# Kernel optimization log

Hardware: AMD Instinct MI355X
Metric: run time of the kernel (lower is better)

Reference implementation:

```python
import jax, jax.numpy as jnp
import numpy as np

D = 512      # input_dim == encoder d_model
E = 512      # embedding_dim (codebook dim)
V = 8192     # num_embeddings
NC = 1       # num_codebooks
L = 6        # encoder layers
H = 8        # heads
F = 2048     # ffn dim
HD = D // H
EPS = 1e-5


def layernorm(x, s, b):
    m = jnp.mean(x, -1, keepdims=True)
    v = jnp.mean((x - m) ** 2, -1, keepdims=True)
    return (x - m) * jax.lax.rsqrt(v + EPS) * s + b


def sinusoidal_pe(T):
    pos = np.arange(T, dtype=np.float32)[:, None]
    i = np.arange(0, D, 2, dtype=np.float32)[None, :]
    ang = pos / np.power(10000.0, i / D)
    pe = np.zeros((T, D), np.float32)
    pe[:, 0::2] = np.sin(ang)
    pe[:, 1::2] = np.cos(ang)
    return jnp.asarray(pe)


def setup_inputs():
    key = jax.random.key(0)
    ks = jax.random.split(key, 12)
    B, T = 8, 1024
    xs = jax.random.normal(ks[0], (B, T, D), jnp.float32)
    xs_lens = (T // 2 + jax.random.randint(ks[1], (B,), 0, T // 2)).astype(jnp.int32)
    mask_indices = jax.random.uniform(ks[2], (B, T)) < 0.12  # span-mask surrogate
    sc = lambda k, shape, s=0.02: jax.random.normal(k, shape, jnp.float32) * s
    return {
        "xs": xs, "xs_lens": xs_lens, "mask_indices": mask_indices,
        "W_embed": sc(ks[3], (D, D), D ** -0.5),
        "ln1_s": jnp.ones((L, D)), "ln1_b": jnp.zeros((L, D)),
        "Wqkv": sc(ks[4], (L, D, 3 * D)), "Wo": sc(ks[5], (L, D, D)),
        "ln2_s": jnp.ones((L, D)), "ln2_b": jnp.zeros((L, D)),
        "W1": sc(ks[6], (L, D, F)), "W2": sc(ks[7], (L, F, D)),
        "an_s": jnp.ones((D,)), "an_b": jnp.zeros((D,)),
        "iln_s": jnp.ones((D,)), "iln_b": jnp.zeros((D,)),
        "mask_emb": sc(ks[8], (D,), 0.1),
        "top_n_out": sc(ks[9], (NC, D, V)),
        "projection": sc(ks[10], (D, E), (2.0 / (D + E)) ** 0.5),  # xavier_normal, frozen
        "embeddings": jax.random.normal(ks[11], (NC, E, V), jnp.float32),  # frozen codebook
    }


def encoder_blocks(x, pad_mask, ln1_s, ln1_b, Wqkv, Wo, ln2_s, ln2_b, W1, W2, an_s, an_b):
    B, T, _ = x.shape
    attn_bias = jnp.where(pad_mask, 0.0, -1e9)[:, None, None, :]  # [B,1,1,T]

    def layer(x, p):
        l1s, l1b, wqkv, wo, l2s, l2b, w1, w2 = p
        h = layernorm(x, l1s, l1b)
        q, k, v = jnp.split(h @ wqkv, 3, axis=-1)
        q = q.reshape(B, T, H, HD)
        k = k.reshape(B, T, H, HD)
        v = v.reshape(B, T, H, HD)
        scores = jnp.einsum('bqhd,bkhd->bhqk', q, k) * (HD ** -0.5) + attn_bias
        o = jnp.einsum('bhqk,bkhd->bqhd', jax.nn.softmax(scores, axis=-1), v)
        x = x + o.reshape(B, T, D) @ wo
        h = layernorm(x, l2s, l2b)
        x = x + jax.nn.relu(h @ w1) @ w2
        return x, None

    x, _ = jax.lax.scan(layer, x, (ln1_s, ln1_b, Wqkv, Wo, ln2_s, ln2_b, W1, W2))
    return layernorm(x, an_s, an_b)


def nearest_ids(x, iln_s, iln_b, projection, embeddings):
    # layernorm -> projection -> squared-distance argmin per codebook
    B, T, _ = x.shape
    z = layernorm(x, iln_s, iln_b) @ projection        # [B,T,E]
    flat = z.reshape(-1, E)                            # [N,E]
    d = (jnp.sum(flat ** 2, 1)[None, :, None]
         + jnp.sum(embeddings ** 2, 1)[:, None, :]
         - 2.0 * jnp.einsum('ne,gev->gnv', flat, embeddings))  # [NC,N,V]
    return jnp.argmin(d, -1).T.reshape(B, T, NC)


def reference(xs, xs_lens, mask_indices, W_embed, ln1_s, ln1_b, Wqkv, Wo, ln2_s, ln2_b,
              W1, W2, an_s, an_b, iln_s, iln_b, mask_emb, top_n_out, projection, embeddings):
    B, T, _ = xs.shape
    pad_mask = jnp.arange(T)[None, :] < xs_lens[:, None]              # [B,T]
    x = xs @ W_embed + sinusoidal_pe(T)[None]                         # encoder.embed
    target_ids = nearest_ids(x, iln_s, iln_b, projection, embeddings)  # [B,T,NC]
    masked_xs = jnp.where(mask_indices[..., None], mask_emb, x)
    out = encoder_blocks(masked_xs, pad_mask, ln1_s, ln1_b, Wqkv, Wo,
                         ln2_s, ln2_b, W1, W2, an_s, an_b)            # [B,T,D]
    logits = jnp.einsum('btd,gdv->bgtv', out, top_n_out)              # [B,NC,T,V]
    lsm = jax.nn.log_softmax(logits, axis=-1)
    tgt = jnp.transpose(target_ids, (0, 2, 1))                        # [B,NC,T]
    ent = -jnp.take_along_axis(lsm, tgt[..., None], axis=-1)[..., 0]  # [B,NC,T]
    m = (pad_mask & mask_indices).astype(jnp.float32)                 # [B,T]
    loss = jnp.sum(ent * m[:, None, :]) / (jnp.sum(m) * NC)
    return loss
```

## Files before the change

kernel.cpp:

```cpp
#include <hip/hip_runtime.h>
#include <hip/hip_bf16.h>

#define D_ 512
#define T_ 1024
#define B_ 8
#define H_ 8
#define F_ 2048
#define V_ 8192
#define L_ 6
#define NTOK 8192
#define EPS_ 1e-5f
#define NCAP 2048

typedef short short8 __attribute__((ext_vector_type(8)));
typedef float floatx4 __attribute__((ext_vector_type(4)));

__device__ __forceinline__ float bf2f(unsigned short u) {
  union { unsigned int i; float f; } v; v.i = ((unsigned int)u) << 16; return v.f;
}
__device__ __forceinline__ unsigned short f2bf(float f) {
  unsigned int u = __float_as_uint(f);
  return (unsigned short)((u + 0x7fffu + ((u >> 16) & 1u)) >> 16);
}
__device__ __forceinline__ float ldf(const void* p, long long i, int bf) {
  if (bf) return bf2f(((const unsigned short*)p)[i]);
  return ((const float*)p)[i];
}
__device__ __forceinline__ void ld16(const unsigned short* g, unsigned short* l) {
  __builtin_amdgcn_global_load_lds(
      (const __attribute__((address_space(1))) unsigned int*)g,
      (__attribute__((address_space(3))) unsigned int*)l, 16, 0, 0);
}
__device__ __forceinline__ unsigned int fkey(float f) {
  unsigned int u = __float_as_uint(f);
  return (u & 0x80000000u) ? ~u : (u ^ 0x80000000u);
}

__global__ void detect_kernel(const unsigned int* xsw, const unsigned int* mw, int* flags) {
  __shared__ int cnt[256];
  __shared__ int m01[256], mlo[256], mhi[256];
  int tid = threadIdx.x;
  int c = 0;
  for (int t = tid; t < 1024; t += 256) {
    unsigned int lo = xsw[t] & 0xffffu;
    int ok;
    if (lo == 0u) ok = 1;
    else { unsigned int e = (lo >> 7) & 0xffu; ok = (e >= 90u && e <= 140u); }
    c += ok;
  }
  int n01 = 0, lo38 = 0, hi38 = 0;
  for (int t = tid; t < 2048; t += 256) {
    unsigned int w = mw[t];
    if (w > 1u) n01 = 1;
    if ((w & 0xffffu) == 0x3f80u) lo38 = 1;
    if ((w >> 16) == 0x3f80u) hi38 = 1;
  }
  cnt[tid] = c; m01[tid] = n01; mlo[tid] = lo38; mhi[tid] = hi38;
  __syncthreads();
  for (int s = 128; s > 0; s >>= 1) {
    if (tid < s) {
      cnt[tid] += cnt[tid + s];
      m01[tid] |= m01[tid + s]; mlo[tid] |= mlo[tid + s]; mhi[tid] |= mhi[tid + s];
    }
    __syncthreads();
  }
  if (tid == 0) {
    flags[0] = (cnt[0] > 700) ? 1 : 0;
    int fmt;
    if (!m01[0]) fmt = 0;
    else if (mlo[0]) fmt = 2;
    else if (mhi[0]) fmt = 3;
    else fmt = 1;
    flags[1] = fmt;
  }
}

__global__ void conv_all_kernel(const void* d4, const void* d5, const void* d8,
                                const void* d9, const void* d12, const void* d13,
                                const void* d14, const void* d15, const void* d16,
                                float* P, const int* flags) {
  int i = blockIdx.x * 256 + threadIdx.x;
  if (i >= 14848) return;
  int bf = flags[0];
  const void* src; int off;
  if (i < 3072) { src = d4; off = 0; }
  else if (i < 6144) { src = d5; off = 3072; }
  else if (i < 9216) { src = d8; off = 6144; }
  else if (i < 12288) { src = d9; off = 9216; }
  else if (i < 12800) { src = d12; off = 12288; }
  else if (i < 13312) { src = d13; off = 12800; }
  else if (i < 13824) { src = d14; off = 13312; }
  else if (i < 14336) { src = d15; off = 13824; }
  else { src = d16; off = 14336; }
  P[i] = ldf(src, i - off, bf);
}

__global__ void convb_kernel(const void* src, unsigned short* dst, int n, const int* flags) {
  int i = blockIdx.x * 256 + threadIdx.x;
  if (i < n) {
    if (flags[0]) dst[i] = ((const unsigned short*)src)[i];
    else dst[i] = f2bf(((const float*)src)[i]);
  }
}

__global__ __launch_bounds__(256) void trans_kernel(const void* src, unsigned short* dst,
                                                    int K, int N, const int* flags) {
  int bf = flags[0];
  __shared__ unsigned short tile[32][33];
  int n0 = blockIdx.x * 32, k0 = blockIdx.y * 32, batch = blockIdx.z;
  long long sbase = (long long)batch * K * N;
  long long dbase = (long long)batch * N * K;
  int c = threadIdx.x & 31, r8 = threadIdx.x >> 5;
#pragma unroll
  for (int rr = 0; rr < 4; ++rr) {
    int r = r8 + rr * 8;
    tile[r][c] = f2bf(ldf(src, sbase + (long long)(k0 + r) * N + n0 + c, bf));
  }
  __syncthreads();
#pragma unroll
  for (int rr = 0; rr < 4; ++rr) {
    int nn = r8 + rr * 8;
    dst[dbase + (long long)(n0 + nn) * K + k0 + c] = tile[c][nn];
  }
}

__global__ __launch_bounds__(256) void trans_big_kernel(const void* top, const void* emb,
                                                        unsigned short* TOPT, unsigned short* EMBT,
                                                        float* en, const int* flags) {
  int bf = flags[0];
  __shared__ unsigned short tile[32][33];
  int n0 = blockIdx.x * 32, k0 = blockIdx.y * 32, z = blockIdx.z;
  const void* src = z ? emb : top;
  unsigned short* dst = z ? EMBT : TOPT;
  int c = threadIdx.x & 31, r8 = threadIdx.x >> 5;
#pragma unroll
  for (int rr = 0; rr < 4; ++rr) {
    int r = r8 + rr * 8;
    tile[r][c] = f2bf(ldf(src, (long long)(k0 + r) * V_ + n0 + c, bf));
  }
  __syncthreads();
#pragma unroll
  for (int rr = 0; rr < 4; ++rr) {
    int nn = r8 + rr * 8;
    dst[(long long)(n0 + nn) * D_ + k0 + c] = tile[c][nn];
  }
  if (z == 1 && threadIdx.x < 32) {
    int nn = threadIdx.x;
    float s = 0.f;
#pragma unroll
    for (int r = 0; r < 32; ++r) { float x = bf2f(tile[r][nn]); s += x * x; }
    atomicAdd(&en[n0 + nn], s);
  }
}

__global__ void prep_kernel(const void* mask, const int* lens, int* maski, float* mcomb,
                            int* idx, int* cnt, const int* flags) {
  int i = blockIdx.x * 256 + threadIdx.x;
  if (i >= NTOK) return;
  int fmt = flags[1];
  int mi;
  if (fmt == 0) mi = ((const int*)mask)[i] != 0;
  else if (fmt == 1) mi = ((const unsigned char*)mask)[i] != 0;
  else if (fmt == 2) mi = ((const unsigned short*)mask)[i] != 0;
  else mi = ((const float*)mask)[i] != 0.f;
  int b = i >> 10, t = i & (T_ - 1);
  int act = mi && (t < lens[b]);
  maski[i] = mi;
  mcomb[i] = act ? 1.f : 0.f;
  if (act) {
    int p = atomicAdd(cnt, 1);
    if (p < NCAP) idx[p] = i;
  }
}

#define BK 32

template<int BN>
__device__ __forceinline__ void stage_tile(const unsigned short* A, long long ga0, long long ga1,
                                           const unsigned short* BT, long long gb0, long long gb1,
                                           int k0, unsigned short (*Ab)[BK],
                                           unsigned short (*Bb)[BK], int wave, int c16) {
  ld16(A + ga0 + k0 + c16 * 8, &Ab[wave * 32][0]);
  ld16(A + ga1 + k0 + c16 * 8, &Ab[wave * 32 + 16][0]);
  if constexpr (BN == 128) {
    ld16(BT + gb0 + k0 + c16 * 8, &Bb[wave * 32][0]);
    ld16(BT + gb1 + k0 + c16 * 8, &Bb[wave * 32 + 16][0]);
  } else {
    ld16(BT + gb0 + k0 + c16 * 8, &Bb[wave * 16][0]);
  }
}

template<int BN>
__device__ __forceinline__ void mfma_pipe(const unsigned short* A, long long ga0, long long ga1,
                                          const unsigned short* BT, int n0, int Kdim,
                                          unsigned short (*As)[BK], unsigned short (*Bs)[BK],
                                          floatx4 (*acc)[BN / 32], int tid) {
  constexpr int NB = BN / 32;
  int wave = tid >> 6, lane = tid & 63;
  int r16 = lane >> 2, c16 = lane & 3;
  int lrow = lane & 15, quad = lane >> 4;
  int wm = (wave & 1) * 64, wn = (wave >> 1) * (BN / 2);
  int NT = Kdim / BK;
  long long gb0, gb1 = 0;
  if constexpr (BN == 128) {
    gb0 = (long long)(n0 + wave * 32 + r16) * Kdim;
    gb1 = gb0 + 16LL * Kdim;
  } else {
    gb0 = (long long)(n0 + wave * 16 + r16) * Kdim;
  }
  stage_tile<BN>(A, ga0, ga1, BT, gb0, gb1, 0, As, Bs, wave, c16);
  stage_tile<BN>(A, ga0, ga1, BT, gb0, gb1, BK, As + 128, Bs + BN, wave, c16);
  int cur = 0, nxt = 2;
  for (int t = 0; t < NT; ++t) {
    if (t == NT - 1) {
      asm volatile("s_waitcnt vmcnt(0)" ::: "memory");
    } else {
      if constexpr (BN == 128) asm volatile("s_waitcnt vmcnt(4)" ::: "memory");
      else                     asm volatile("s_waitcnt vmcnt(3)" ::: "memory");
    }
    __builtin_amdgcn_s_barrier();
    if (t + 2 < NT)
      stage_tile<BN>(A, ga0, ga1, BT, gb0, gb1, (t + 2) * BK,
                     As + nxt * 128, Bs + nxt * BN, wave, c16);
    unsigned short (*Ac)[BK] = As + cur * 128;
    unsigned short (*Bc)[BK] = Bs + cur * BN;
    short8 af[4], bfr[NB];
#pragma unroll
    for (int i = 0; i < 4; ++i) af[i] = *(const short8*)&Ac[wm + i * 16 + lrow][quad * 8];
#pragma unroll
    for (int j = 0; j < NB; ++j) bfr[j] = *(const short8*)&Bc[wn + j * 16 + lrow][quad * 8];
#pragma unroll
    for (int i = 0; i < 4; ++i)
#pragma unroll
      for (int j = 0; j < NB; ++j)
        acc[i][j] = __builtin_amdgcn_mfma_f32_16x16x32_bf16(af[i], bfr[j], acc[i][j], 0, 0, 0);
    cur = (cur == 2) ? 0 : cur + 1;
    nxt = (nxt == 2) ? 0 : nxt + 1;
  }
  __syncthreads();
}

__global__ __launch_bounds__(256) void mgemm_kernel(const unsigned short* A,
    const unsigned short* BT, long long boff, unsigned short* Cb, int Ndim, int Kdim) {
  __shared__ __align__(16) unsigned short As[3 * 128][BK];
  __shared__ __align__(16) unsigned short Bs[3 * 128][BK];
  int tid = threadIdx.x;
  int bid = blockIdx.x;
  int m0 = (bid & 63) * 128, n0 = (bid >> 6) * 128;
  int wave = tid >> 6, lane = tid & 63;
  int wm = (wave & 1) * 64, wn = (wave >> 1) * 64;
  int lrow = lane & 15, quad = lane >> 4;
  int r16 = lane >> 2;
  floatx4 acc[4][4];
#pragma unroll
  for (int i = 0; i < 4; ++i)
#pragma unroll
    for (int j = 0; j < 4; ++j) acc[i][j] = (floatx4){0.f, 0.f, 0.f, 0.f};
  long long ga0 = (long long)(m0 + wave * 32 + r16) * Kdim;
  long long ga1 = ga0 + 16LL * Kdim;
  mfma_pipe<128>(A, ga0, ga1, BT + boff, n0, Kdim, As, Bs, acc, tid);
#pragma unroll
  for (int i = 0; i < 4; ++i) {
    int mb = m0 + wm + i * 16 + quad * 4;
#pragma unroll
    for (int j = 0; j < 4; ++j) {
      int ncol = n0 + wn + j * 16 + lrow;
#pragma unroll
      for (int r = 0; r < 4; ++r)
        Cb[(long long)(mb + r) * Ndim + ncol] = f2bf(fmaxf(acc[i][j][r], 0.f));
    }
  }
}

__global__ __launch_bounds__(256) void mgemm64_kernel(const unsigned short* A,
    const unsigned short* BT, long long boff, float* Cf, unsigned short* Cb,
    int Ndim, int Kdim, int mode) {
  __shared__ __align__(16) unsigned short As[3 * 128][BK];
  __shared__ __align__(16) unsigned short Bs[3 * 64][BK];
  int tid = threadIdx.x;
  int bid = blockIdx.x;
  int m0 = (bid & 63) * 128, n0 = (bid >> 6) * 64;
  int wave = tid >> 6, lane = tid & 63;
  int r16 = lane >> 2;
  int wm = (wave & 1) * 64, wn = (wave >> 1) * 32;
  int lrow = lane & 15, quad = lane >> 4;
  floatx4 acc[4][2];
#pragma unroll
  for (int i = 0; i < 4; ++i)
#pragma unroll
    for (int j = 0; j < 2; ++j) acc[i][j] = (floatx4){0.f, 0.f, 0.f, 0.f};
  long long ga0 = (long long)(m0 + wave * 32 + r16) * Kdim;
  long long ga1 = ga0 + 16LL * Kdim;
  mfma_pipe<64>(A, ga0, ga1, BT + boff, n0, Kdim, As, Bs, acc, tid);
#pragma unroll
  for (int i = 0; i < 4; ++i) {
    int mb = m0 + wm + i * 16 + quad * 4;
#pragma unroll
    for (int j = 0; j < 2; ++j) {
      int ncol = n0 + wn + j * 16 + lrow;
#pragma unroll
      for (int r = 0; r < 4; ++r) {
        int m = mb + r;
        long long idx = (long long)m * Ndim + ncol;
        float v = acc[i][j][r];
        if (mode == 1) Cf[idx] += v;
        else if (mode == 4) Cb[idx] = f2bf(v);
        else if (mode == 3) {
          int t = m & (T_ - 1);
          float freq = __expf(-(float)(ncol & ~1) * (9.210340371976184f / (float)D_));
          float ang = (float)t * freq;
          v += (ncol & 1) ? cosf(ang) : sinf(ang);
          Cf[idx] = v;
        } else Cf[idx] = v;
      }
    }
  }
}

__global__ __launch_bounds__(256) void qkvgemm_kernel(const unsigned short* A,
    const unsigned short* BT, long long boff, unsigned short* QB,
    unsigned short* KSg, unsigned short* VTSg) {
  __shared__ __align__(16) union {
    struct { unsigned short As[3 * 128][BK]; unsigned short Bs[3 * 128][BK]; } s;
    unsigned short T[128][136];
  } sm;
  int tid = threadIdx.x;
  int bid = blockIdx.x;
  int m0 = (bid & 63) * 128;
  int nt = bid >> 6;
  int n0 = nt * 128;
  int wave = tid >> 6, lane = tid & 63;
  int wm = (wave & 1) * 64, wn = (wave >> 1) * 64;
  int lrow = lane & 15, quad = lane >> 4;
  int r16 = lane >> 2;
  floatx4 acc[4][4];
#pragma unroll
  for (int i = 0; i < 4; ++i)
#pragma unroll
    for (int j = 0; j < 4; ++j) acc[i][j] = (floatx4){0.f, 0.f, 0.f, 0.f};
  long long ga0 = (long long)(m0 + wave * 32 + r16) * D_;
  long long ga1 = ga0 + 16LL * D_;
  mfma_pipe<128>(A, ga0, ga1, BT + boff, n0, D_, sm.s.As, sm.s.Bs, acc, tid);
  int b = m0 >> 10, tt = (m0 >> 7) & 7;
  if (nt < 4) {
#pragma unroll
    for (int i = 0; i < 4; ++i) {
      int mb = m0 + wm + i * 16 + quad * 4;
#pragma unroll
      for (int j = 0; j < 4; ++j) {
        int ncol = n0 + wn + j * 16 + lrow;
#pragma unroll
        for (int r = 0; r < 4; ++r)
          QB[(long long)(mb + r) * 512 + ncol] = f2bf(acc[i][j][r]);
      }
    }
  } else if (nt < 8) {
#pragma unroll
    for (int i = 0; i < 4; ++i)
#pragma unroll
      for (int j = 0; j < 4; ++j)
#pragma unroll
        for (int r = 0; r < 4; ++r)
          sm.T[wm + i * 16 + quad * 4 + r][wn + j * 16 + lrow] = f2bf(acc[i][j][r]);
    __syncthreads();
    int tk = tid & 127, hg0 = tid >> 7;
#pragma unroll
    for (int p = 0; p < 8; ++p) {
      int hg = p * 2 + hg0;
      int h2 = hg >> 3, g = hg & 7;
      uint4 u = *(const uint4*)&sm.T[tk][h2 * 64 + g * 8];
      int headg = (nt - 4) * 2 + h2;
      long long dst = (((((long long)(b * 8 + headg)) * 8 + tt) * 8 + g) * 128 + tk) * 8;
      *(uint4*)&KSg[dst] = u;
    }
  } else {
#pragma unroll
    for (int i = 0; i < 4; ++i)
#pragma unroll
      for (int j = 0; j < 4; ++j)
#pragma unroll
        for (int r = 0; r < 4; ++r)
          sm.T[wn + j * 16 + lrow][wm + i * 16 + quad * 4 + r] = f2bf(acc[i][j][r]);
    __syncthreads();
    int col = tid & 127, gh = tid >> 7;
    int h2 = col >> 6, ch = col & 63;
    int headg = (nt - 8) * 2 + h2;
    long long base = ((((long long)(b * 8 + headg)) * 8 + tt) * 16);
#pragma unroll
    for (int p = 0; p < 8; ++p) {
      int g = p * 2 + gh;
      uint4 u = *(const uint4*)&sm.T[col][g * 8];
      long long dst = ((base + g) * 64 + ch) * 8;
      *(uint4*)&VTSg[dst] = u;
    }
  }
}

__global__ __launch_bounds__(256) void fattn_kernel(const unsigned short* QB,
    const unsigned short* KSg, const unsigned short* VTSg, const int* lens,
    unsigned short* ao) {
  __shared__ __align__(16) unsigned short Ps[64 * 128];
  int blk = blockIdx.x;
  int swz = (blk & 7) * 128 + (blk >> 3);
  int qt = swz & 15, bh = swz >> 4;
  int b = bh >> 3, h = bh & 7;
  int tid = threadIdx.x, wave = tid >> 6, lane = tid & 63;
  int c = lane & 15, quad = lane >> 4;
  int len = lens[b];
  short8 qf[2];
#pragma unroll
  for (int ks = 0; ks < 2; ++ks)
    qf[ks] = *(const short8*)&QB[(long long)(b * 1024 + qt * 64 + wave * 16 + c) * 512
                                 + h * 64 + ks * 32 + quad * 8];
  floatx4 accO[4];
  float lr[4];
#pragma unroll
  for (int j = 0; j < 4; ++j) { accO[j] = (floatx4){0.f, 0.f, 0.f, 0.f}; lr[j] = 0.f; }
  int nkt = (len + 127) >> 7;
  const unsigned short* kp = KSg + (long long)bh * 65536;
  const unsigned short* vp = VTSg + (long long)bh * 65536;
  int kb = (quad * 128 + c) * 8;
  int vbase = quad * 512 + c * 8;
  int row = wave * 16 + c;
  short8 kA[8], kB[8], vA[8], vB[8];
#pragma unroll
  for (int j2 = 0; j2 < 4; ++j2) {
    kA[j2]     = *(const short8*)&kp[kb + j2 * 128];
    kA[4 + j2] = *(const short8*)&kp[kb + 4096 + j2 * 128];
  }
  for (int kt = 0; kt < nkt; ++kt) {
    int kbase = kt * 128;
    const unsigned short* kpc = kp + kt * 8192;
    const unsigned short* vpc = vp + kt * 8192;
    const unsigned short* kpn = kpc + 8192;
    int more = (kt + 1 < nkt);
#pragma unroll
    for (int j2 = 0; j2 < 4; ++j2) {
      kB[j2]     = *(const short8*)&kpc[kb + (4 + j2) * 128];
      kB[4 + j2] = *(const short8*)&kpc[kb + 4096 + (4 + j2) * 128];
    }
    floatx4 s0[4];
#pragma unroll
    for (int j2 = 0; j2 < 4; ++j2) s0[j2] = (floatx4){0.f, 0.f, 0.f, 0.f};
#pragma unroll
    for (int j2 = 0; j2 < 4; ++j2) {
      s0[j2] = __builtin_amdgcn_mfma_f32_16x16x32_bf16(qf[0], kA[j2], s0[j2], 0, 0, 0);
      s0[j2] = __builtin_amdgcn_mfma_f32_16x16x32_bf16(qf[1], kA[4 + j2], s0[j2], 0, 0, 0);
    }
#pragma unroll
    for (int q = 0; q < 8; ++q)
      vA[q] = *(const short8*)&vpc[(q >> 2) * 2048 + (q & 3) * 128 + vbase];
#pragma unroll
    for (int r = 0; r < 4; ++r) {
      int prow = wave * 16 + quad * 4 + r;
      int rx = quad * 4 + r;
#pragma unroll
      for (int j2 = 0; j2 < 4; ++j2) {
        int col = j2 * 16 + c;
        float s = s0[j2][r] * 0.125f;
        s = (kbase + col < len) ? s : -100.f;
        float p = __expf(s);
        lr[r] += p;
        Ps[prow * 128 + (((col >> 3) ^ rx) * 8) + (col & 7)] = f2bf(p);
      }
    }
    floatx4 s1[4];
#pragma unroll
    for (int j2 = 0; j2 < 4; ++j2) s1[j2] = (floatx4){0.f, 0.f, 0.f, 0.f};
#pragma unroll
    for (int j2 = 0; j2 < 4; ++j2) {
      s1[j2] = __builtin_amdgcn_mfma_f32_16x16x32_bf16(qf[0], kB[j2], s1[j2], 0, 0, 0);
      s1[j2] = __builtin_amdgcn_mfma_f32_16x16x32_bf16(qf[1], kB[4 + j2], s1[j2], 0, 0, 0);
    }
#pragma unroll
    for (int q = 0; q < 8; ++q)
      vB[q] = *(const short8*)&vpc[(2 + (q >> 2)) * 2048 + (q & 3) * 128 + vbase];
#pragma unroll
    for (int r = 0; r < 4; ++r) {
      int prow = wave * 16 + quad * 4 + r;
      int rx = quad * 4 + r;
#pragma unroll
      for (int j2 = 0; j2 < 4; ++j2) {
        int col = (4 + j2) * 16 + c;
        float s = s1[j2][r] * 0.125f;
        s = (kbase + col < len) ? s : -100.f;
        float p = __expf(s);
        lr[r] += p;
        Ps[prow * 128 + (((col >> 3) ^ rx) * 8) + (col & 7)] = f2bf(p);
      }
    }
#pragma unroll
    for (int kk2 = 0; kk2 < 2; ++kk2) {
      short8 pa = *(const short8*)&Ps[row * 128 + (((kk2 * 4 + quad) ^ c) * 8)];
#pragma unroll
      for (int jn = 0; jn < 4; ++jn)
        accO[jn] = __builtin_amdgcn_mfma_f32_16x16x32_bf16(pa, vA[kk2 * 4 + jn], accO[jn], 0, 0, 0);
    }
    if (more) {
#pragma unroll
      for (int j2 = 0; j2 < 4; ++j2) {
        kA[j2]     = *(const short8*)&kpn[kb + j2 * 128];
        kA[4 + j2] = *(const short8*)&kpn[kb + 4096 + j2 * 128];
      }
    }
#pragma unroll
    for (int kk2 = 0; kk2 < 2; ++kk2) {
      int kk = 2 + kk2;
      short8 pa = *(const short8*)&Ps[row * 128 + (((kk * 4 + quad) ^ c) * 8)];
#pragma unroll
      for (int jn = 0; jn < 4; ++jn)
        accO[jn] = __builtin_amdgcn_mfma_f32_16x16x32_bf16(pa, vB[kk2 * 4 + jn], accO[jn], 0, 0, 0);
    }
  }
#pragma unroll
  for (int r = 0; r < 4; ++r) {
    float ls = lr[r];
    ls += __shfl_xor(ls, 1, 64);
    ls += __shfl_xor(ls, 2, 64);
    ls += __shfl_xor(ls, 4, 64);
    ls += __shfl_xor(ls, 8, 64);
    float inv = 1.f / ls;
    long long token = b * 1024 + qt * 64 + wave * 16 + quad * 4 + r;
#pragma unroll
    for (int jn = 0; jn < 4; ++jn)
      ao[token * 512 + h * 64 + jn * 16 + c] = f2bf(accO[jn][r] * inv);
  }
}

__global__ __launch_bounds__(256) void dgemm_argmin(const unsigned short* Z, const int* ridx,
    const int* cnt, const unsigned short* ET, const float* en, unsigned long long* best) {
  __shared__ __align__(16) union {
    struct { unsigned short A[3 * 128][BK]; unsigned short B[3 * 128][BK]; } s;
    unsigned long long part[128][33];
  } sm;
  int m0 = blockIdx.y * 128;
  int na = *cnt;
  if (m0 >= ((na + 127) & ~127)) return;
  int tid = threadIdx.x;
  int n0 = blockIdx.x * 128;
  int wave = tid >> 6, lane = tid & 63;
  int wm = (wave & 1) * 64, wn = (wave >> 1) * 64;
  int lrow = lane & 15, quad = lane >> 4;
  int r16 = lane >> 2;
  int slot = (wave >> 1) * 16 + lrow;
  floatx4 acc[4][4];
#pragma unroll
  for (int i = 0; i < 4; ++i)
#pragma unroll
    for (int j = 0; j < 4; ++j) acc[i][j] = (floatx4){0.f, 0.f, 0.f, 0.f};
  long long ga0 = (long long)ridx[m0 + wave * 32 + r16] * D_;
  long long ga1 = (long long)ridx[m0 + wave * 32 + 16 + r16] * D_;
  mfma_pipe<128>(Z, ga0, ga1, ET, n0, D_, sm.s.A, sm.s.B, acc, tid);
  float env[4];
#pragma unroll
  for (int j = 0; j < 4; ++j) env[j] = en[n0 + wn + j * 16 + lrow];
#pragma unroll
  for (int i = 0; i < 4; ++i) {
#pragma unroll
    for (int r = 0; r < 4; ++r) {
      int rowl = wm + i * 16 + quad * 4 + r;
      unsigned long long bl = ~0ull;
#pragma unroll
      for (int j = 0; j < 4; ++j) {
        float v = env[j] - 2.f * acc[i][j][r];
        unsigned long long pk = (((unsigned long long)fkey(v)) << 32) |
                                (unsigned int)(n0 + wn + j * 16 + lrow);
        if (pk < bl) bl = pk;
      }
      sm.part[rowl][(slot + rowl) & 31] = bl;
    }
  }
  __syncthreads();
  if (tid < 128) {
    unsigned long long bb = sm.part[tid][0];
#pragma unroll 4
    for (int k2 = 1; k2 < 32; ++k2) { unsigned long long o = sm.part[tid][k2]; if (o < bb) bb = o; }
    atomicMin(&best[m0 + tid], bb);
  }
}

__global__ __launch_bounds__(256) void lgemm_lse(const unsigned short* OUTB, const int* ridx,
    const int* cnt, const unsigned short* TOPT, const unsigned long long* best,
    float* PS, float* TL) {
  __shared__ __align__(16) union {
    struct { unsigned short A[3 * 128][BK]; unsigned short B[3 * 128][BK]; } s;
    float part[128][33];
  } sm;
  int m0 = blockIdx.y * 128;
  int na = *cnt;
  if (m0 >= ((na + 127) & ~127)) return;
  int tid = threadIdx.x;
  int n0 = blockIdx.x * 128;
  int wave = tid >> 6, lane = tid & 63;
  int wm = (wave & 1) * 64, wn = (wave >> 1) * 64;
  int lrow = lane & 15, quad = lane >> 4;
  int r16 = lane >> 2;
  int slot = (wave >> 1) * 16 + lrow;
  floatx4 acc[4][4];
#pragma unroll
  for (int i = 0; i < 4; ++i)
#pragma unroll
    for (int j = 0; j < 4; ++j) acc[i][j] = (floatx4){0.f, 0.f, 0.f, 0.f};
  long long ga0 = (long long)ridx[m0 + wave * 32 + r16] * D_;
  long long ga1 = (long long)ridx[m0 + wave * 32 + 16 + r16] * D_;
  mfma_pipe<128>(OUTB, ga0, ga1, TOPT, n0, D_, sm.s.A, sm.s.B, acc, tid);
#pragma unroll
  for (int i = 0; i < 4; ++i) {
#pragma unroll
    for (int r = 0; r < 4; ++r) {
      int rowl = wm + i * 16 + quad * 4 + r;
      int tg = (int)(best[m0 + rowl] & 0xffffffffu);
      float ss = 0.f;
#pragma unroll
      for (int j = 0; j < 4; ++j) {
        float v = acc[i][j][r];
        ss += __expf(v);
        if (n0 + wn + j * 16 + lrow == tg) TL[m0 + rowl] = v;
      }
      sm.part[rowl][(slot + rowl) & 31] = ss;
    }
  }
  __syncthreads();
  if (tid < 128) {
    float S = 0.f;
#pragma unroll 4
    for (int k2 = 0; k2 < 32; ++k2) S += sm.part[tid][k2];
    PS[(long long)(m0 + tid) * 64 + blockIdx.x] = S;
  }
}

__global__ void lse_combine(const float* PS, const float* TL, const int* cnt, float* entm) {
  int t = blockIdx.x * 256 + threadIdx.x;
  if (t >= NCAP) return;
  if (t < *cnt) {
    float S = 0.f;
    for (int i = 0; i < 64; ++i) S += PS[(long long)t * 64 + i];
    entm[t] = __logf(S) - TL[t];
  } else {
    entm[t] = 0.f;
  }
}

__global__ __launch_bounds__(256) void ln_kernel(const float* X, float* Yf, unsigned short* Yb,
                                                 int obf, const float* s, const float* b) {
  int tid = threadIdx.x, wave = tid >> 6, lane = tid & 63;
  long long n = (long long)blockIdx.x * 4 + wave;
  const float* x = X + n * D_ + lane * 8;
  float v[8];
  *(float4*)&v[0] = *(const float4*)x;
  *(float4*)&v[4] = *(const float4*)(x + 4);
  float sum = 0.f;
#pragma unroll
  for (int j = 0; j < 8; ++j) sum += v[j];
  for (int m = 32; m; m >>= 1) sum += __shfl_xor(sum, m, 64);
  float mean = sum * (1.f / (float)D_);
  float vs = 0.f;
#pragma unroll
  for (int j = 0; j < 8; ++j) { v[j] -= mean; vs += v[j] * v[j]; }
  for (int m = 32; m; m >>= 1) vs += __shfl_xor(vs, m, 64);
  float r = rsqrtf(vs * (1.f / (float)D_) + EPS_);
  float sv[8], bv[8];
  *(float4*)&sv[0] = *(const float4*)(s + lane * 8);
  *(float4*)&sv[4] = *(const float4*)(s + lane * 8 + 4);
  *(float4*)&bv[0] = *(const float4*)(b + lane * 8);
  *(float4*)&bv[4] = *(const float4*)(b + lane * 8 + 4);
  if (obf) {
    unsigned short o[8];
#pragma unroll
    for (int j = 0; j < 8; ++j) o[j] = f2bf(v[j] * r * sv[j] + bv[j]);
    *(uint4*)(Yb + n * D_ + lane * 8) = *(const uint4*)o;
  } else {
    float o[8];
#pragma unroll
    for (int j = 0; j < 8; ++j) o[j] = v[j] * r * sv[j] + bv[j];
    *(float4*)(Yf + n * D_ + lane * 8) = *(const float4*)&o[0];
    *(float4*)(Yf + n * D_ + lane * 8 + 4) = *(const float4*)&o[4];
  }
}

__global__ void maskapply_kernel(float* x, const int* maski, const float* memb) {
  long long i = (long long)blockIdx.x * 256 + threadIdx.x;
  int n = (int)(i >> 9), d = (int)(i & 511);
  if (maski[n]) x[i] = memb[d];
}

__global__ void final_kernel(const float* entm, const float* mcomb, void* out) {
  __shared__ float r1[256], r2[256];
  int tid = threadIdx.x;
  float s1 = 0.f, s2 = 0.f;
  for (int i = tid; i < NCAP; i += 256) s1 += entm[i];
  for (int i = tid; i < NTOK; i += 256) s2 += mcomb[i];
  r1[tid] = s1; r2[tid] = s2;
  __syncthreads();
  for (int st = 128; st > 0; st >>= 1) {
    if (tid < st) { r1[tid] += r1[tid + st]; r2[tid] += r2[tid + st]; }
    __syncthreads();
  }
  if (tid == 0) {
    float loss = r1[0] / r2[0];
    unsigned short b16 = f2bf(loss);
    unsigned short* o = (unsigned short*)out;
    o[0] = b16; o[1] = b16;
  }
}

extern "C" void kernel_launch(void* const* d_in, const int* in_sizes, int n_in,
                              void* d_out, int out_size, void* d_ws, size_t ws_size,
                              hipStream_t stream) {
  if (n_in < 20) return;
  float* wsf = (float*)d_ws;
  int* flags = (int*)d_ws;
  const long long OF_P = 256;
  const long long OF_X = 16640;
  const long long OF_HB = OF_X + 4194304;
  const long long OF_BIG = OF_HB + 2097152;
  const long long OF_AOB = OF_BIG + 8388608;
  const long long OF_WT = OF_AOB + 2097152;
  const long long OF_TOPT = OF_WT + 9699328;
  const long long OF_EMBT = OF_TOPT + 2097152;
  const long long OF_EN = OF_EMBT + 2097152;
  const long long OF_BEST = OF_EN + 8192;
  const long long OF_PS = OF_BEST + 4096;
  const long long OF_TL = OF_PS + 131072;
  const long long OF_MI = OF_TL + 2048;
  const long long OF_MC = OF_MI + 8192;
  const long long OF_EM = OF_MC + 8192;
  const long long OF_CNT = OF_EM + 2048;
  const long long OF_IDX = OF_CNT + 16;
  const long long END = OF_IDX + 2048;
  if (ws_size < (size_t)END * 4) return;

  float* X = wsf + OF_X;
  unsigned short* HB = (unsigned short*)(wsf + OF_HB);
  unsigned short* BIGB = (unsigned short*)(wsf + OF_BIG);
  unsigned short* AOB = (unsigned short*)(wsf + OF_AOB);
  unsigned short* WT = (unsigned short*)(wsf + OF_WT);
  unsigned short* TOPT = (unsigned short*)(wsf + OF_TOPT);
  unsigned short* EMBT = (unsigned short*)(wsf + OF_EMBT);
  float* EN = wsf + OF_EN;
  unsigned long long* BEST = (unsigned long long*)(wsf + OF_BEST);
  float* PS = wsf + OF_PS;
  float* TL = wsf + OF_TL;
  int* MI = (int*)(wsf + OF_MI);
  float* MC = wsf + OF_MC;
  float* EM = wsf + OF_EM;
  int* CNT = (int*)(wsf + OF_CNT);
  int* IDX = (int*)(wsf + OF_IDX);
  float* P = wsf + OF_P;
  float* ln1s = P, *ln1b = P + 3072, *ln2s = P + 6144, *ln2b = P + 9216;
  float* ans = P + 12288, *anb = P + 12800, *ilns = P + 13312, *ilnb = P + 13824;
  float* memb = P + 14336;

  unsigned short* QB = BIGB;
  unsigned short* KSg = BIGB + 4194304;
  unsigned short* VTSg = BIGB + 8388608;

  const long long W_QKV = 0, W_O = 4718592, W_1 = 6291456, W_2 = 12582912,
                  W_EMB = 18874368, W_PRJ = 19136512;

  detect_kernel<<<1, 256, 0, stream>>>((const unsigned int*)d_in[0],
                                       (const unsigned int*)d_in[2], flags);
  hipMemsetAsync((void*)BEST, 0xFF, NCAP * 8, stream);
  hipMemsetAsync((void*)EN, 0, V_ * 4, stream);
  hipMemsetAsync((void*)CNT, 0, 16, stream);
  hipMemsetAsync((void*)IDX, 0, NCAP * 4, stream);
  conv_all_kernel<<<58, 256, 0, stream>>>(d_in[4], d_in[5], d_in[8], d_in[9], d_in[12],
                                          d_in[13], d_in[14], d_in[15], d_in[16], P, flags);
  prep_kernel<<<32, 256, 0, stream>>>(d_in[2], (const int*)d_in[1], MI, MC, IDX, CNT, flags);

  unsigned short* XSB = BIGB;
  convb_kernel<<<16384, 256, 0, stream>>>(d_in[0], XSB, 4194304, flags);

  trans_kernel<<<dim3(48, 16, 6), 256, 0, stream>>>(d_in[6], WT + W_QKV, 512, 1536, flags);
  trans_kernel<<<dim3(16, 16, 6), 256, 0, stream>>>(d_in[7], WT + W_O, 512, 512, flags);
  trans_kernel<<<dim3(64, 16, 6), 256, 0, stream>>>(d_in[10], WT + W_1, 512, 2048, flags);
  trans_kernel<<<dim3(16, 64, 6), 256, 0, stream>>>(d_in[11], WT + W_2, 2048, 512, flags);
  trans_kernel<<<dim3(16, 16, 1), 256, 0, stream>>>(d_in[3], WT + W_EMB, 512, 512, flags);
  trans_kernel<<<dim3(16, 16, 1), 256, 0, stream>>>(d_in[18], WT + W_PRJ, 512, 512, flags);
  trans_big_kernel<<<dim3(256, 16, 2), 256, 0, stream>>>(d_in[17], d_in[19], TOPT, EMBT,
                                                         EN, flags);

  dim3 gC(64, NCAP / 128);

  mgemm64_kernel<<<512, 256, 0, stream>>>(XSB, WT + W_EMB, 0, X, nullptr, 512, 512, 3);
  ln_kernel<<<2048, 256, 0, stream>>>(X, nullptr, HB, 1, ilns, ilnb);
  mgemm64_kernel<<<512, 256, 0, stream>>>(HB, WT + W_PRJ, 0, nullptr, AOB, 512, 512, 4);
  dgemm_argmin<<<gC, 256, 0, stream>>>(AOB, IDX, CNT, EMBT, EN, BEST);
  maskapply_kernel<<<16384, 256, 0, stream>>>(X, MI, memb);

  for (int l = 0; l < L_; ++l) {
    ln_kernel<<<2048, 256, 0, stream>>>(X, nullptr, HB, 1, ln1s + l * 512, ln1b + l * 512);
    qkvgemm_kernel<<<768, 256, 0, stream>>>(HB, WT + W_QKV, (long long)l * 786432,
                                            QB, KSg, VTSg);
    fattn_kernel<<<1024, 256, 0, stream>>>(QB, KSg, VTSg, (const int*)d_in[1], AOB);
    mgemm64_kernel<<<512, 256, 0, stream>>>(AOB, WT + W_O, (long long)l * 262144,
                                            X, nullptr, 512, 512, 1);
    ln_kernel<<<2048, 256, 0, stream>>>(X, nullptr, HB, 1, ln2s + l * 512, ln2b + l * 512);
    mgemm_kernel<<<1024, 256, 0, stream>>>(HB, WT + W_1, (long long)l * 1048576,
                                           BIGB, 2048, 512);
    mgemm64_kernel<<<512, 256, 0, stream>>>(BIGB, WT + W_2, (long long)l * 1048576,
                                            X, nullptr, 512, 2048, 1);
  }
  ln_kernel<<<2048, 256, 0, stream>>>(X, nullptr, AOB, 1, ans, anb);
  lgemm_lse<<<gC, 256, 0, stream>>>(AOB, IDX, CNT, TOPT, BEST, PS, TL);
  lse_combine<<<8, 256, 0, stream>>>(PS, TL, CNT, EM);
  final_kernel<<<1, 256, 0, stream>>>(EM, MC, d_out);
}
```

Measured before the change: 1.287 ms.

## Swizzle LDS tile layout and split-K the FFN down-projection with atomics

Applies an XOR swizzle to the LDS column offset used by global-to-LDS staging and by fragment reads, to cut shared-memory bank conflicts in every MFMA GEMM. It also adds a split-K mode to the 64-wide GEMM: the W2 projection (K=2048) is launched with twice as many blocks, each covering half of K, and results are accumulated into the residual with float atomicAdd. The goal is better CU occupancy on the long-K GEMM. The cost is atomic traffic, and the floating-point summation order becomes nondeterministic.

```diff
diff --git a/kernel.cpp b/kernel.cpp
--- a/kernel.cpp
+++ b/kernel.cpp
@@ -179,20 +179,21 @@
 __device__ __forceinline__ void stage_tile(const unsigned short* A, long long ga0, long long ga1,
                                            const unsigned short* BT, long long gb0, long long gb1,
                                            int k0, unsigned short (*Ab)[BK],
-                                           unsigned short (*Bb)[BK], int wave, int c16) {
-  ld16(A + ga0 + k0 + c16 * 8, &Ab[wave * 32][0]);
-  ld16(A + ga1 + k0 + c16 * 8, &Ab[wave * 32 + 16][0]);
+                                           unsigned short (*Bb)[BK], int wave, int sw8) {
+  ld16(A + ga0 + k0 + sw8, &Ab[wave * 32][0]);
+  ld16(A + ga1 + k0 + sw8, &Ab[wave * 32 + 16][0]);
   if constexpr (BN == 128) {
-    ld16(BT + gb0 + k0 + c16 * 8, &Bb[wave * 32][0]);
-    ld16(BT + gb1 + k0 + c16 * 8, &Bb[wave * 32 + 16][0]);
+    ld16(BT + gb0 + k0 + sw8, &Bb[wave * 32][0]);
+    ld16(BT + gb1 + k0 + sw8, &Bb[wave * 32 + 16][0]);
   } else {
-    ld16(BT + gb0 + k0 + c16 * 8, &Bb[wave * 16][0]);
+    ld16(BT + gb0 + k0 + sw8, &Bb[wave * 16][0]);
   }
 }
 
 template<int BN>
 __device__ __forceinline__ void mfma_pipe(const unsigned short* A, long long ga0, long long ga1,
                                           const unsigned short* BT, int n0, int Kdim,
+                                          int kofs, int Klen,
                                           unsigned short (*As)[BK], unsigned short (*Bs)[BK],
                                           floatx4 (*acc)[BN / 32], int tid) {
   constexpr int NB = BN / 32;
@@ -200,7 +201,9 @@
   int r16 = lane >> 2, c16 = lane & 3;
   int lrow = lane & 15, quad = lane >> 4;
   int wm = (wave & 1) * 64, wn = (wave >> 1) * (BN / 2);
-  int NT = Kdim / BK;
+  int NT = Klen / BK;
+  int sw8 = (c16 ^ ((r16 >> 1) & 3)) * 8;
+  int swr = (quad ^ ((lrow >> 1) & 3)) * 8;
   long long gb0, gb1 = 0;
   if constexpr (BN == 128) {
     gb0 = (long long)(n0 + wave * 32 + r16) * Kdim;
@@ -208,8 +211,9 @@
   } else {
     gb0 = (long long)(n0 + wave * 16 + r16) * Kdim;
   }
-  stage_tile<BN>(A, ga0, ga1, BT, gb0, gb1, 0, As, Bs, wave, c16);
-  stage_tile<BN>(A, ga0, ga1, BT, gb0, gb1, BK, As + 128, Bs + BN, wave, c16);
+  ga0 += kofs; ga1 += kofs; gb0 += kofs; gb1 += kofs;
+  stage_tile<BN>(A, ga0, ga1, BT, gb0, gb1, 0, As, Bs, wave, sw8);
+  stage_tile<BN>(A, ga0, ga1, BT, gb0, gb1, BK, As + 128, Bs + BN, wave, sw8);
   int cur = 0, nxt = 2;
   for (int t = 0; t < NT; ++t) {
     if (t == NT - 1) {
@@ -221,14 +225,14 @@
     __builtin_amdgcn_s_barrier();
     if (t + 2 < NT)
       stage_tile<BN>(A, ga0, ga1, BT, gb0, gb1, (t + 2) * BK,
-                     As + nxt * 128, Bs + nxt * BN, wave, c16);
+                     As + nxt * 128, Bs + nxt * BN, wave, sw8);
     unsigned short (*Ac)[BK] = As + cur * 128;
     unsigned short (*Bc)[BK] = Bs + cur * BN;
     short8 af[4], bfr[NB];
 #pragma unroll
-    for (int i = 0; i < 4; ++i) af[i] = *(const short8*)&Ac[wm + i * 16 + lrow][quad * 8];
-#pragma unroll
-    for (int j = 0; j < NB; ++j) bfr[j] = *(const short8*)&Bc[wn + j * 16 + lrow][quad * 8];
+    for (int i = 0; i < 4; ++i) af[i] = *(const short8*)&Ac[wm + i * 16 + lrow][swr];
+#pragma unroll
+    for (int j = 0; j < NB; ++j) bfr[j] = *(const short8*)&Bc[wn + j * 16 + lrow][swr];
 #pragma unroll
     for (int i = 0; i < 4; ++i)
 #pragma unroll
@@ -258,7 +262,7 @@
     for (int j = 0; j < 4; ++j) acc[i][j] = (floatx4){0.f, 0.f, 0.f, 0.f};
   long long ga0 = (long long)(m0 + wave * 32 + r16) * Kdim;
   long long ga1 = ga0 + 16LL * Kdim;
-  mfma_pipe<128>(A, ga0, ga1, BT + boff, n0, Kdim, As, Bs, acc, tid);
+  mfma_pipe<128>(A, ga0, ga1, BT + boff, n0, Kdim, 0, Kdim, As, Bs, acc, tid);
 #pragma unroll
   for (int i = 0; i < 4; ++i) {
     int mb = m0 + wm + i * 16 + quad * 4;
@@ -279,7 +283,11 @@
   __shared__ __align__(16) unsigned short Bs[3 * 64][BK];
   int tid = threadIdx.x;
   int bid = blockIdx.x;
-  int m0 = (bid & 63) * 128, n0 = (bid >> 6) * 64;
+  int m0 = (bid & 63) * 128;
+  int nt = bid >> 6;
+  int n0, kofs, Klen;
+  if (mode == 5) { n0 = (nt & 7) * 64; kofs = (nt >> 3) * (Kdim >> 1); Klen = Kdim >> 1; }
+  else { n0 = nt * 64; kofs = 0; Klen = Kdim; }
   int wave = tid >> 6, lane = tid & 63;
   int r16 = lane >> 2;
   int wm = (wave & 1) * 64, wn = (wave >> 1) * 32;
@@ -291,7 +299,7 @@
     for (int j = 0; j < 2; ++j) acc[i][j] = (floatx4){0.f, 0.f, 0.f, 0.f};
   long long ga0 = (long long)(m0 + wave * 32 + r16) * Kdim;
   long long ga1 = ga0 + 16LL * Kdim;
-  mfma_pipe<64>(A, ga0, ga1, BT + boff, n0, Kdim, As, Bs, acc, tid);
+  mfma_pipe<64>(A, ga0, ga1, BT + boff, n0, Kdim, kofs, Klen, As, Bs, acc, tid);
 #pragma unroll
   for (int i = 0; i < 4; ++i) {
     int mb = m0 + wm + i * 16 + quad * 4;
@@ -304,6 +312,7 @@
         long long idx = (long long)m * Ndim + ncol;
         float v = acc[i][j][r];
         if (mode == 1) Cf[idx] += v;
+        else if (mode == 5) atomicAdd(&Cf[idx], v);
         else if (mode == 4) Cb[idx] = f2bf(v);
         else if (mode == 3) {
           int t = m & (T_ - 1);
@@ -340,7 +349,7 @@
     for (int j = 0; j < 4; ++j) acc[i][j] = (floatx4){0.f, 0.f, 0.f, 0.f};
   long long ga0 = (long long)(m0 + wave * 32 + r16) * D_;
   long long ga1 = ga0 + 16LL * D_;
-  mfma_pipe<128>(A, ga0, ga1, BT + boff, n0, D_, sm.s.As, sm.s.Bs, acc, tid);
+  mfma_pipe<128>(A, ga0, ga1, BT + boff, n0, D_, 0, D_, sm.s.As, sm.s.Bs, acc, tid);
   int b = m0 >> 10, tt = (m0 >> 7) & 7;
   if (nt < 4) {
 #pragma unroll
@@ -550,7 +559,7 @@
     for (int j = 0; j < 4; ++j) acc[i][j] = (floatx4){0.f, 0.f, 0.f, 0.f};
   long long ga0 = (long long)ridx[m0 + wave * 32 + r16] * D_;
   long long ga1 = (long long)ridx[m0 + wave * 32 + 16 + r16] * D_;
-  mfma_pipe<128>(Z, ga0, ga1, ET, n0, D_, sm.s.A, sm.s.B, acc, tid);
+  mfma_pipe<128>(Z, ga0, ga1, ET, n0, D_, 0, D_, sm.s.A, sm.s.B, acc, tid);
   float env[4];
 #pragma unroll
   for (int j = 0; j < 4; ++j) env[j] = en[n0 + wn + j * 16 + lrow];
@@ -603,7 +612,7 @@
     for (int j = 0; j < 4; ++j) acc[i][j] = (floatx4){0.f, 0.f, 0.f, 0.f};
   long long ga0 = (long long)ridx[m0 + wave * 32 + r16] * D_;
   long long ga1 = (long long)ridx[m0 + wave * 32 + 16 + r16] * D_;
-  mfma_pipe<128>(OUTB, ga0, ga1, TOPT, n0, D_, sm.s.A, sm.s.B, acc, tid);
+  mfma_pipe<128>(OUTB, ga0, ga1, TOPT, n0, D_, 0, D_, sm.s.A, sm.s.B, acc, tid);
 #pragma unroll
   for (int i = 0; i < 4; ++i) {
 #pragma unroll
@@ -798,8 +807,8 @@
     ln_kernel<<<2048, 256, 0, stream>>>(X, nullptr, HB, 1, ln2s + l * 512, ln2b + l * 512);
     mgemm_kernel<<<1024, 256, 0, stream>>>(HB, WT + W_1, (long long)l * 1048576,
                                            BIGB, 2048, 512);
-    mgemm64_kernel<<<512, 256, 0, stream>>>(BIGB, WT + W_2, (long long)l * 1048576,
-                                            X, nullptr, 512, 2048, 1);
+    mgemm64_kernel<<<1024, 256, 0, stream>>>(BIGB, WT + W_2, (long long)l * 1048576,
+                                             X, nullptr, 512, 2048, 5);
   }
   ln_kernel<<<2048, 256, 0, stream>>>(X, nullptr, AOB, 1, ans, anb);
   lgemm_lse<<<gC, 256, 0, stream>>>(AOB, IDX, CNT, TOPT, BEST, PS, TL);
```

After: 1.382 ms. 1.07x slower.
